# Optimization experiments

Hardware: AMD Instinct MI355X
Metric: run time of the kernel (lower is better)

## Reference

```python
import jax, jax.numpy as jnp
import numpy as np

N = 4096            # tokens (dim 0 of x)
LATENT = 1024       # latent_vector_size
H = 16              # num_heads
DK = 64             # key_dim
DV = 64             # val_dim
MHK = H * DK        # 1024, width of q and k blocks


def setup_inputs() -> dict:
    key = jax.random.key(0)
    ks = jax.random.split(key, 5)
    return {
        "x": jax.random.normal(ks[0], (N, LATENT), dtype=jnp.float32),
        "w_qkv": jax.random.normal(ks[1], (LATENT, H * (2 * DK + DV)), dtype=jnp.float32) * (1.0 / np.sqrt(LATENT)),
        "b_qkv": jax.random.normal(ks[2], (H * (2 * DK + DV),), dtype=jnp.float32) * 0.01,
        "w_out": jax.random.normal(ks[3], (H * DV, LATENT), dtype=jnp.float32) * (1.0 / np.sqrt(H * DV)),
        "b_out": jax.random.normal(ks[4], (LATENT,), dtype=jnp.float32) * 0.01,
    }


def reference(x, w_qkv, b_qkv, w_out, b_out):
    # qkv projection: [N, H*(2*Dk+Dv)]
    qkv = x @ w_qkv + b_qkv
    # NOTE: the original module does NOT split into heads; q/k/v are the
    # concatenated head dims and a single [N, N] score matrix is formed,
    # scaled by sqrt(key_dim) (per-head dim), not sqrt(H*key_dim).
    q = qkv[:, :MHK]                 # [N, H*Dk]
    k = qkv[:, MHK:2 * MHK]          # [N, H*Dk]
    v = qkv[:, 2 * MHK:]             # [N, H*Dv]
    scores = (q @ k.T) * (1.0 / jnp.sqrt(jnp.float32(DK)))  # [N, N]
    attn = jax.nn.softmax(scores, axis=-1)
    out = attn @ v                   # [N, H*Dv]
    return out @ w_out + b_out       # [N, LATENT]
```

## Files before the change

### kernel.cpp

```cpp
#include <hip/hip_runtime.h>
#include <hip/hip_fp16.h>


typedef _Float16 half_t;
typedef _Float16 half8 __attribute__((ext_vector_type(8)));
typedef _Float16 half4 __attribute__((ext_vector_type(4)));
typedef float f32x4 __attribute__((ext_vector_type(4)));

static constexpr int N_TOK = 4096;
static constexpr int LATENT = 1024;
static constexpr int QKVN = 3072;

#define DEVI __device__ __forceinline__

DEVI void gld_lds16(const half_t* g, half_t* l) {
  __builtin_amdgcn_global_load_lds(
      (const __attribute__((address_space(1))) void*)g,
      (__attribute__((address_space(3))) void*)l,
      16, 0, 0);
}

DEVI f32x4 MFMA(half8 a, half8 b, f32x4 c) {
  return __builtin_amdgcn_mfma_f32_16x16x32_f16(a, b, c, 0, 0, 0);
}


DEVI void stageH(const half_t* __restrict__ g, int ld, half_t* lbase, int tid) {
#pragma unroll
  for (int i = 0; i < 2; ++i) {
    int c = tid + i * 512;
    int r = c >> 2;
    int k8 = ((c & 3) ^ ((r >> 1) & 3)) * 8;
    gld_lds16(g + (size_t)r * ld + k8, lbase + c * 8);
  }
}

template <int MODE>
__launch_bounds__(512, 2)
__global__ void gemm8(const half_t* __restrict__ A, int lda,
                      const half_t* __restrict__ B, int ldb,
                      void* __restrict__ Cout, int ldc,
                      const float* __restrict__ bias, int K) {
  __shared__ half_t Alds[2][2][256 * 32];
  __shared__ half_t Blds[2][2][256 * 32];

  const int tid = threadIdx.x;
  const int lane = tid & 63;
  const int wid = tid >> 6;

  const int nx = gridDim.x;
  const int nwg = nx * gridDim.y;
  const int bid = blockIdx.y * nx + blockIdx.x;
  const int cpx = nwg >> 3;
  const int swz = (bid & 7) * cpx + (bid >> 3);
  const int rowBlk = (swz / nx) * 256;
  const int colBlk = (swz % nx) * 256;

  const int wr = (wid >> 2) * 128;
  const int wc = (wid & 3) * 64;
  const int fr = lane & 15;
  const int fs = lane >> 4;

  const int kOff = blockIdx.z * K;
  const half_t* Ag = A + (size_t)rowBlk * lda + kOff;
  const half_t* Bg = B + (size_t)colBlk * ldb + kOff;

  f32x4 acc[8][4] = {};
  const int NT = K >> 6;

  stageH(Ag, lda, Alds[0][0], tid);
  stageH(Bg, ldb, Blds[0][0], tid);
  stageH(Ag + 32, lda, Alds[0][1], tid);
  stageH(Bg + 32, ldb, Blds[0][1], tid);
  asm volatile("s_waitcnt vmcnt(4)" ::: "memory");
  __builtin_amdgcn_s_barrier();

  for (int kt = 0; kt < NT; ++kt) {
    const int b = kt & 1;
    const bool st = (kt + 1 < NT);
    const half_t* AgN = Ag + (kt + 1) * 64;
    const half_t* BgN = Bg + (kt + 1) * 64;

    half8 af[8], bf[4];

#pragma unroll
    for (int kh = 0; kh < 2; ++kh) {
      const half_t* Ac = Alds[b][kh];
      const half_t* Bc = Blds[b][kh];
#pragma unroll
      for (int m = 0; m < 8; ++m) {
        int row = wr + m * 16 + fr;
        af[m] = *(const half8*)(Ac + row * 32 + ((fs ^ ((row >> 1) & 3)) * 8));
      }
#pragma unroll
      for (int n = 0; n < 4; ++n) {
        int row = wc + n * 16 + fr;
        bf[n] = *(const half8*)(Bc + row * 32 + ((fs ^ ((row >> 1) & 3)) * 8));
      }
      if (st) {
        stageH(AgN + kh * 32, lda, Alds[b ^ 1][kh], tid);
        stageH(BgN + kh * 32, ldb, Blds[b ^ 1][kh], tid);
      }
      __builtin_amdgcn_s_barrier();
      __builtin_amdgcn_s_setprio(1);
#pragma unroll
      for (int m = 0; m < 8; ++m)
#pragma unroll
        for (int n = 0; n < 4; ++n)
          acc[m][n] = MFMA(af[m], bf[n], acc[m][n]);
      __builtin_amdgcn_s_setprio(0);
      if (st) asm volatile("s_waitcnt vmcnt(4)" ::: "memory");
      else if (kh == 0) asm volatile("s_waitcnt vmcnt(0)" ::: "memory");
      __builtin_amdgcn_s_barrier();
    }
  }

  const size_t zoff = (MODE == 2) ? (size_t)blockIdx.z * N_TOK * ldc : 0;
#pragma unroll
  for (int m = 0; m < 8; ++m) {
#pragma unroll
    for (int n = 0; n < 4; ++n) {
#pragma unroll
      for (int j = 0; j < 4; ++j) {
        int row = rowBlk + wr + m * 16 + (lane >> 4) * 4 + j;
        int col = colBlk + wc + n * 16 + fr;
        float v = acc[m][n][j];
        if (MODE == 0) {
          v += bias[col];
          if (col < 1024) v *= 0.125f;
          ((half_t*)Cout)[(size_t)row * ldc + col] = (half_t)v;
        } else if (MODE == 1) {
          ((half_t*)Cout)[(size_t)row * ldc + col] = (half_t)v;
        } else {
          ((half_t*)Cout)[zoff + (size_t)row * ldc + col] = (half_t)v;
        }
      }
    }
  }
}

template <int ROWS>
DEVI void stage32(const half_t* __restrict__ g, int ld, half_t* lbase, int tid) {
#pragma unroll
  for (int c = tid; c < ROWS * 4; c += 256) {
    int r = c >> 2;
    int k8 = ((c & 3) ^ ((r >> 1) & 3)) * 8;
    gld_lds16(g + (size_t)r * ld + k8, lbase + c * 8);
  }
}

__launch_bounds__(256, 2)
__global__ void gemm2(const half_t* __restrict__ A, int lda,
                      const half_t* __restrict__ B, int ldb,
                      half_t* __restrict__ Cout, int ldc, int K) {
  constexpr int BM = 128, BN = 128, MF = 4, NF = 4;
  __shared__ half_t At[2][BM * 32];
  __shared__ half_t Bt[2][BN * 32];

  const int tid = threadIdx.x;
  const int lane = tid & 63;
  const int wid = tid >> 6;

  const int nx = gridDim.x;
  const int nwg = nx * gridDim.y;
  const int bid = blockIdx.y * nx + blockIdx.x;
  const int cpx = nwg >> 3;
  const int swz = (bid & 7) * cpx + (bid >> 3);
  const int rowBlk = (swz / nx) * BM;
  const int colBlk = (swz % nx) * BN;

  const int wr = (wid >> 1) * (BM / 2);
  const int wc = (wid & 1) * (BN / 2);
  const int fr = lane & 15;
  const int fs = lane >> 4;

  const half_t* Ag = A + (size_t)rowBlk * lda;
  const half_t* Bg = B + (size_t)colBlk * ldb;

  f32x4 acc[MF][NF] = {};
  const int NT = K >> 5;
  stage32<BM>(Ag, lda, At[0], tid);
  stage32<BN>(Bg, ldb, Bt[0], tid);
  __syncthreads();

  int cur = 0;
  for (int t = 0; t < NT; ++t) {
    if (t + 1 < NT) {
      stage32<BM>(Ag + (t + 1) * 32, lda, At[cur ^ 1], tid);
      stage32<BN>(Bg + (t + 1) * 32, ldb, Bt[cur ^ 1], tid);
    }
    const half_t* Ac = At[cur];
    const half_t* Bc = Bt[cur];
    half8 af[MF], bf[NF];
#pragma unroll
    for (int m = 0; m < MF; ++m) {
      int row = wr + m * 16 + fr;
      af[m] = *(const half8*)(Ac + row * 32 + ((fs ^ ((row >> 1) & 3)) * 8));
    }
#pragma unroll
    for (int n = 0; n < NF; ++n) {
      int row = wc + n * 16 + fr;
      bf[n] = *(const half8*)(Bc + row * 32 + ((fs ^ ((row >> 1) & 3)) * 8));
    }
#pragma unroll
    for (int m = 0; m < MF; ++m)
#pragma unroll
      for (int n = 0; n < NF; ++n)
        acc[m][n] = MFMA(af[m], bf[n], acc[m][n]);
    __syncthreads();
    cur ^= 1;
  }

#pragma unroll
  for (int m = 0; m < MF; ++m)
#pragma unroll
    for (int n = 0; n < NF; ++n)
#pragma unroll
      for (int j = 0; j < 4; ++j) {
        int row = rowBlk + wr + m * 16 + (lane >> 4) * 4 + j;
        int col = colBlk + wc + n * 16 + fr;
        Cout[(size_t)row * ldc + col] = (half_t)acc[m][n][j];
      }
}

__launch_bounds__(256)
__global__ void reduce_bias4(const half_t* __restrict__ p, const float* __restrict__ bias,
                             float* __restrict__ out) {
  int i = blockIdx.x * 256 + threadIdx.x;
  const size_t stride8 = (size_t)N_TOK * LATENT / 8;
  half8 a = ((const half8*)p)[i];
  half8 b = ((const half8*)p)[i + stride8];
  half8 c = ((const half8*)p)[i + 2 * stride8];
  half8 d = ((const half8*)p)[i + 3 * stride8];
  float4 e0 = ((const float4*)bias)[(i & 127) * 2];
  float4 e1 = ((const float4*)bias)[(i & 127) * 2 + 1];
  float r[8];
#pragma unroll
  for (int j = 0; j < 8; ++j)
    r[j] = (float)a[j] + (float)b[j] + (float)c[j] + (float)d[j];
  float4 o0, o1;
  o0.x = r[0] + e0.x; o0.y = r[1] + e0.y; o0.z = r[2] + e0.z; o0.w = r[3] + e0.w;
  o1.x = r[4] + e1.x; o1.y = r[5] + e1.y; o1.z = r[6] + e1.z; o1.w = r[7] + e1.w;
  ((float4*)out)[i * 2] = o0;
  ((float4*)out)[i * 2 + 1] = o1;
}

__launch_bounds__(256)
__global__ void softmax_rows(const half_t* __restrict__ S, half_t* __restrict__ P) {
  const int row = blockIdx.x;
  const int t = threadIdx.x;
  const half8* s8 = (const half8*)(S + (size_t)row * N_TOK);

  half8 v[2];
  float lmax = -1e30f;
#pragma unroll
  for (int i = 0; i < 2; ++i) {
    v[i] = s8[t + i * 256];
#pragma unroll
    for (int j = 0; j < 8; ++j) lmax = fmaxf(lmax, (float)v[i][j]);
  }
#pragma unroll
  for (int off = 32; off; off >>= 1) lmax = fmaxf(lmax, __shfl_xor(lmax, off));

  __shared__ float redm[4];
  __shared__ float reds[4];
  if ((t & 63) == 0) redm[t >> 6] = lmax;
  __syncthreads();
  lmax = fmaxf(fmaxf(redm[0], redm[1]), fmaxf(redm[2], redm[3]));

  float e[16];
  float lsum = 0.f;
#pragma unroll
  for (int i = 0; i < 2; ++i)
#pragma unroll
    for (int j = 0; j < 8; ++j) {
      float ev = __expf((float)v[i][j] - lmax);
      e[i * 8 + j] = ev;
      lsum += ev;
    }
#pragma unroll
  for (int off = 32; off; off >>= 1) lsum += __shfl_xor(lsum, off);
  if ((t & 63) == 0) reds[t >> 6] = lsum;
  __syncthreads();
  float inv = 1.f / (reds[0] + reds[1] + reds[2] + reds[3]);

  half8* p8 = (half8*)(P + (size_t)row * N_TOK);
#pragma unroll
  for (int i = 0; i < 2; ++i) {
    half8 h;
#pragma unroll
    for (int j = 0; j < 8; ++j) h[j] = (half_t)(e[i * 8 + j] * inv);
    p8[t + i * 256] = h;
  }
}

template <typename TI>
__global__ void transpose_to_f16(const TI* __restrict__ in, int ldin,
                                 half_t* __restrict__ out, int ldout) {
  __shared__ float tile[32][33];
  const int cb = blockIdx.x * 32;
  const int rb = blockIdx.y * 32;
  const int tx = threadIdx.x;
#pragma unroll
  for (int i = threadIdx.y; i < 32; i += 8)
    tile[i][tx] = (float)in[(size_t)(rb + i) * ldin + cb + tx];
  __syncthreads();
#pragma unroll
  for (int i = threadIdx.y; i < 32; i += 8)
    out[(size_t)(cb + i) * ldout + rb + tx] = (half_t)tile[tx][i];
}

__global__ void cvt_f32_f16(const float* __restrict__ in, half_t* __restrict__ out) {
  int i = blockIdx.x * 256 + threadIdx.x;
  float4 v = ((const float4*)in)[i];
  half4 h;
  h[0] = (half_t)v.x; h[1] = (half_t)v.y; h[2] = (half_t)v.z; h[3] = (half_t)v.w;
  ((half4*)out)[i] = h;
}

extern "C" void kernel_launch(void* const* d_in, const int* in_sizes, int n_in,
                              void* d_out, int out_size, void* d_ws, size_t ws_size,
                              hipStream_t stream) {
  const float* x = (const float*)d_in[0];
  const float* w_qkv = (const float*)d_in[1];
  const float* b_qkv = (const float*)d_in[2];
  const float* w_out = (const float*)d_in[3];
  const float* b_out = (const float*)d_in[4];
  float* out = (float*)d_out;

  char* ws = (char*)d_ws;
  half_t* xb    = (half_t*)(ws);
  half_t* wqkvT = (half_t*)(ws + ((size_t)8 << 20));
  half_t* qkv   = (half_t*)(ws + ((size_t)14 << 20));
  half_t* S     = (half_t*)(ws + ((size_t)46 << 20));
  half_t* P     = (half_t*)(ws + ((size_t)78 << 20));
  half_t* vwT   = (half_t*)(ws + ((size_t)118 << 20));
  half_t* woutT = (half_t*)(ws + ((size_t)126 << 20));
  half_t* parts = (half_t*)(ws + ((size_t)14 << 20));

  dim3 tb(32, 8);

  cvt_f32_f16<<<(N_TOK * LATENT) / (256 * 4), 256, 0, stream>>>(x, xb);
  transpose_to_f16<float><<<dim3(QKVN / 32, LATENT / 32), tb, 0, stream>>>(w_qkv, QKVN, wqkvT, LATENT);
  transpose_to_f16<float><<<dim3(LATENT / 32, LATENT / 32), tb, 0, stream>>>(w_out, LATENT, woutT, LATENT);
  gemm8<0><<<dim3(QKVN / 256, N_TOK / 256), 512, 0, stream>>>(
      xb, LATENT, wqkvT, LATENT, qkv, QKVN, b_qkv, LATENT);
  gemm2<<<dim3(N_TOK / 128, LATENT / 128), 256, 0, stream>>>(
      woutT, LATENT, qkv + 2 * LATENT, QKVN, vwT, N_TOK, LATENT);
  gemm8<1><<<dim3(N_TOK / 256, N_TOK / 256), 512, 0, stream>>>(
      qkv, QKVN, qkv + LATENT, QKVN, S, N_TOK, nullptr, LATENT);
  softmax_rows<<<N_TOK, 256, 0, stream>>>(S, P);
  gemm8<2><<<dim3(LATENT / 256, N_TOK / 256, 4), 512, 0, stream>>>(
      P, N_TOK, vwT, N_TOK, parts, LATENT, nullptr, 1024);
  reduce_bias4<<<(N_TOK * LATENT) / (256 * 8), 256, 0, stream>>>(parts, b_out, out);
}
```

Before: 172.6 us.

## Fuse softmax into score GEMM epilogue and PV GEMM prologue

Removes the standalone softmax pass. The score GEMM epilogue now computes per-tile row max and sum-exp partials, a small combine kernel merges them into a per-row max and inverse sum, and the PV GEMM exponentiates and normalizes the raw scores as it loads A fragments from LDS. This avoids reading S and writing P through global memory, at the cost of recomputing exp2 in the PV GEMM's inner loop, where each A element is exponentiated once per column-block workgroup (four times per element). It also adds register pressure and VALU work between the LDS reads and the MFMAs.

```diff
diff --git a/kernel.cpp b/kernel.cpp
--- a/kernel.cpp
+++ b/kernel.cpp
@@ -10,8 +10,12 @@
 static constexpr int N_TOK = 4096;
 static constexpr int LATENT = 1024;
 static constexpr int QKVN = 3072;
+static constexpr float LOG2E = 1.44269504f;
 
 #define DEVI __device__ __forceinline__
+#define BAR() __builtin_amdgcn_s_barrier()
+#define PRIO(x) __builtin_amdgcn_s_setprio(x)
+#define VMCNT(n) asm volatile("s_waitcnt vmcnt(" #n ")" ::: "memory")
 
 DEVI void gld_lds16(const half_t* g, half_t* l) {
   __builtin_amdgcn_global_load_lds(
@@ -37,10 +41,13 @@
 
 template <int MODE>
 __launch_bounds__(512, 2)
-__global__ void gemm8(const half_t* __restrict__ A, int lda,
-                      const half_t* __restrict__ B, int ldb,
-                      void* __restrict__ Cout, int ldc,
-                      const float* __restrict__ bias, int K) {
+__global__ void gemm8h(const half_t* __restrict__ A, int lda,
+                       const half_t* __restrict__ B, int ldb,
+                       void* __restrict__ Cout, int ldc,
+                       const float* __restrict__ bias, int K,
+                       float2* __restrict__ partials,
+                       const float* __restrict__ mstar,
+                       const float* __restrict__ linv) {
   __shared__ half_t Alds[2][2][256 * 32];
   __shared__ half_t Blds[2][2][256 * 32];
 
@@ -65,6 +72,16 @@
   const half_t* Ag = A + (size_t)rowBlk * lda + kOff;
   const half_t* Bg = B + (size_t)colBlk * ldb + kOff;
 
+  float mrow[8], irow[8];
+  if (MODE == 2) {
+#pragma unroll
+    for (int mm = 0; mm < 8; ++mm) {
+      int r = rowBlk + wr + mm * 16 + fr;
+      mrow[mm] = mstar[r];
+      irow[mm] = linv[r];
+    }
+  }
+
   f32x4 acc[8][4] = {};
   const int NT = K >> 6;
 
@@ -72,8 +89,8 @@
   stageH(Bg, ldb, Blds[0][0], tid);
   stageH(Ag + 32, lda, Alds[0][1], tid);
   stageH(Bg + 32, ldb, Blds[0][1], tid);
-  asm volatile("s_waitcnt vmcnt(4)" ::: "memory");
-  __builtin_amdgcn_s_barrier();
+  VMCNT(4);
+  BAR();
 
   for (int kt = 0; kt < NT; ++kt) {
     const int b = kt & 1;
@@ -82,7 +99,6 @@
     const half_t* BgN = Bg + (kt + 1) * 64;
 
     half8 af[8], bf[4];
-
 #pragma unroll
     for (int kh = 0; kh < 2; ++kh) {
       const half_t* Ac = Alds[b][kh];
@@ -92,6 +108,15 @@
         int row = wr + m * 16 + fr;
         af[m] = *(const half8*)(Ac + row * 32 + ((fs ^ ((row >> 1) & 3)) * 8));
       }
+      if (MODE == 2) {
+#pragma unroll
+        for (int m = 0; m < 8; ++m)
+#pragma unroll
+          for (int e = 0; e < 8; ++e) {
+            float s = (float)af[m][e];
+            af[m][e] = (half_t)(exp2f(s * LOG2E - mrow[m]) * irow[m]);
+          }
+      }
 #pragma unroll
       for (int n = 0; n < 4; ++n) {
         int row = wc + n * 16 + fr;
@@ -101,17 +126,17 @@
         stageH(AgN + kh * 32, lda, Alds[b ^ 1][kh], tid);
         stageH(BgN + kh * 32, ldb, Blds[b ^ 1][kh], tid);
       }
-      __builtin_amdgcn_s_barrier();
-      __builtin_amdgcn_s_setprio(1);
+      BAR();
+      PRIO(1);
 #pragma unroll
       for (int m = 0; m < 8; ++m)
 #pragma unroll
         for (int n = 0; n < 4; ++n)
           acc[m][n] = MFMA(af[m], bf[n], acc[m][n]);
-      __builtin_amdgcn_s_setprio(0);
-      if (st) asm volatile("s_waitcnt vmcnt(4)" ::: "memory");
-      else if (kh == 0) asm volatile("s_waitcnt vmcnt(0)" ::: "memory");
-      __builtin_amdgcn_s_barrier();
+      PRIO(0);
+      if (st) VMCNT(4);
+      else if (kh == 0) VMCNT(0);
+      BAR();
     }
   }
 
@@ -137,6 +162,63 @@
       }
     }
   }
+
+  if (MODE == 1) {
+    float* sM = (float*)&Alds[0][0][0];
+    float* sL = sM + 4 * 256;
+    const int nq = wid & 3;
+    const int g = lane >> 4;
+#pragma unroll
+    for (int m = 0; m < 8; ++m) {
+#pragma unroll
+      for (int j = 0; j < 4; ++j) {
+        float vmax = -1e30f;
+#pragma unroll
+        for (int n = 0; n < 4; ++n) vmax = fmaxf(vmax, acc[m][n][j]);
+#pragma unroll
+        for (int off = 1; off <= 8; off <<= 1) vmax = fmaxf(vmax, __shfl_xor(vmax, off));
+        float vsum = 0.f;
+#pragma unroll
+        for (int n = 0; n < 4; ++n) vsum += __expf(acc[m][n][j] - vmax);
+#pragma unroll
+        for (int off = 1; off <= 8; off <<= 1) vsum += __shfl_xor(vsum, off);
+        if (fr == 0) {
+          int rl = wr + m * 16 + g * 4 + j;
+          sM[nq * 256 + rl] = vmax;
+          sL[nq * 256 + rl] = vsum;
+        }
+      }
+    }
+    BAR();
+    if (tid < 256) {
+      float m0 = sM[tid], m1 = sM[256 + tid], m2 = sM[512 + tid], m3 = sM[768 + tid];
+      float mb = fmaxf(fmaxf(m0, m1), fmaxf(m2, m3));
+      float lb = sL[tid] * __expf(m0 - mb) + sL[256 + tid] * __expf(m1 - mb) +
+                 sL[512 + tid] * __expf(m2 - mb) + sL[768 + tid] * __expf(m3 - mb);
+      float2 st;
+      st.x = mb;
+      st.y = lb;
+      partials[(size_t)(rowBlk + tid) * 16 + (swz % nx)] = st;
+    }
+  }
+}
+
+__launch_bounds__(256)
+__global__ void combine_stats(const float2* __restrict__ partials,
+                              float* __restrict__ mstar, float* __restrict__ linv) {
+  int row = blockIdx.x * 256 + threadIdx.x;
+  float2 p[16];
+  float m = -1e30f;
+#pragma unroll
+  for (int b = 0; b < 16; ++b) {
+    p[b] = partials[(size_t)row * 16 + b];
+    m = fmaxf(m, p[b].x);
+  }
+  float l = 0.f;
+#pragma unroll
+  for (int b = 0; b < 16; ++b) l += p[b].y * __expf(p[b].x - m);
+  mstar[row] = m * LOG2E;
+  linv[row] = 1.f / l;
 }
 
 template <int ROWS>
@@ -245,55 +327,6 @@
   ((float4*)out)[i * 2 + 1] = o1;
 }
 
-__launch_bounds__(256)
-__global__ void softmax_rows(const half_t* __restrict__ S, half_t* __restrict__ P) {
-  const int row = blockIdx.x;
-  const int t = threadIdx.x;
-  const half8* s8 = (const half8*)(S + (size_t)row * N_TOK);
-
-  half8 v[2];
-  float lmax = -1e30f;
-#pragma unroll
-  for (int i = 0; i < 2; ++i) {
-    v[i] = s8[t + i * 256];
-#pragma unroll
-    for (int j = 0; j < 8; ++j) lmax = fmaxf(lmax, (float)v[i][j]);
-  }
-#pragma unroll
-  for (int off = 32; off; off >>= 1) lmax = fmaxf(lmax, __shfl_xor(lmax, off));
-
-  __shared__ float redm[4];
-  __shared__ float reds[4];
-  if ((t & 63) == 0) redm[t >> 6] = lmax;
-  __syncthreads();
-  lmax = fmaxf(fmaxf(redm[0], redm[1]), fmaxf(redm[2], redm[3]));
-
-  float e[16];
-  float lsum = 0.f;
-#pragma unroll
-  for (int i = 0; i < 2; ++i)
-#pragma unroll
-    for (int j = 0; j < 8; ++j) {
-      float ev = __expf((float)v[i][j] - lmax);
-      e[i * 8 + j] = ev;
-      lsum += ev;
-    }
-#pragma unroll
-  for (int off = 32; off; off >>= 1) lsum += __shfl_xor(lsum, off);
-  if ((t & 63) == 0) reds[t >> 6] = lsum;
-  __syncthreads();
-  float inv = 1.f / (reds[0] + reds[1] + reds[2] + reds[3]);
-
-  half8* p8 = (half8*)(P + (size_t)row * N_TOK);
-#pragma unroll
-  for (int i = 0; i < 2; ++i) {
-    half8 h;
-#pragma unroll
-    for (int j = 0; j < 8; ++j) h[j] = (half_t)(e[i * 8 + j] * inv);
-    p8[t + i * 256] = h;
-  }
-}
-
 template <typename TI>
 __global__ void transpose_to_f16(const TI* __restrict__ in, int ldin,
                                  half_t* __restrict__ out, int ldout) {
@@ -333,7 +366,9 @@
   half_t* wqkvT = (half_t*)(ws + ((size_t)8 << 20));
   half_t* qkv   = (half_t*)(ws + ((size_t)14 << 20));
   half_t* S     = (half_t*)(ws + ((size_t)46 << 20));
-  half_t* P     = (half_t*)(ws + ((size_t)78 << 20));
+  float2* partials = (float2*)(ws + ((size_t)78 << 20));
+  float*  mstar = (float*)(ws + ((size_t)79 << 20));
+  float*  linv  = (float*)(ws + ((size_t)79 << 20) + 65536);
   half_t* vwT   = (half_t*)(ws + ((size_t)118 << 20));
   half_t* woutT = (half_t*)(ws + ((size_t)126 << 20));
   half_t* parts = (half_t*)(ws + ((size_t)14 << 20));
@@ -343,14 +378,14 @@
   cvt_f32_f16<<<(N_TOK * LATENT) / (256 * 4), 256, 0, stream>>>(x, xb);
   transpose_to_f16<float><<<dim3(QKVN / 32, LATENT / 32), tb, 0, stream>>>(w_qkv, QKVN, wqkvT, LATENT);
   transpose_to_f16<float><<<dim3(LATENT / 32, LATENT / 32), tb, 0, stream>>>(w_out, LATENT, woutT, LATENT);
-  gemm8<0><<<dim3(QKVN / 256, N_TOK / 256), 512, 0, stream>>>(
-      xb, LATENT, wqkvT, LATENT, qkv, QKVN, b_qkv, LATENT);
+  gemm8h<0><<<dim3(QKVN / 256, N_TOK / 256), 512, 0, stream>>>(
+      xb, LATENT, wqkvT, LATENT, qkv, QKVN, b_qkv, LATENT, nullptr, nullptr, nullptr);
   gemm2<<<dim3(N_TOK / 128, LATENT / 128), 256, 0, stream>>>(
       woutT, LATENT, qkv + 2 * LATENT, QKVN, vwT, N_TOK, LATENT);
-  gemm8<1><<<dim3(N_TOK / 256, N_TOK / 256), 512, 0, stream>>>(
-      qkv, QKVN, qkv + LATENT, QKVN, S, N_TOK, nullptr, LATENT);
-  softmax_rows<<<N_TOK, 256, 0, stream>>>(S, P);
-  gemm8<2><<<dim3(LATENT / 256, N_TOK / 256, 4), 512, 0, stream>>>(
-      P, N_TOK, vwT, N_TOK, parts, LATENT, nullptr, 1024);
+  gemm8h<1><<<dim3(N_TOK / 256, N_TOK / 256), 512, 0, stream>>>(
+      qkv, QKVN, qkv + LATENT, QKVN, S, N_TOK, nullptr, LATENT, partials, nullptr, nullptr);
+  combine_stats<<<N_TOK / 256, 256, 0, stream>>>(partials, mstar, linv);
+  gemm8h<2><<<dim3(LATENT / 256, N_TOK / 256, 4), 512, 0, stream>>>(
+      S, N_TOK, vwT, N_TOK, parts, LATENT, nullptr, 1024, nullptr, mstar, linv);
   reduce_bias4<<<(N_TOK * LATENT) / (256 * 8), 256, 0, stream>>>(parts, b_out, out);
 }
```

Result: slower. 238.2 us (+38.0%).
